# Optimization experiments

Hardware: AMD Instinct MI355X
Metric: run time of the kernel (lower is better)

The kernel has to match this reference:

```python
import jax, jax.numpy as jnp
import numpy as np

B, S, E, H, WIN = 2, 2048, 1024, 16, 16
D = E // H  # head dim = 64


def setup_inputs() -> dict:
    key = jax.random.key(0)
    ks = jax.random.split(key, 9)
    s = 0.02
    f32 = jnp.float32
    return {
        "hidden_states": jax.random.normal(ks[0], (B, S, E), f32),
        "in_w_cls": jax.random.normal(ks[1], (3 * E, E), f32) * s,
        "in_b_cls": jnp.zeros((3 * E,), f32),
        "out_w_cls": jax.random.normal(ks[2], (E, E), f32) * s,
        "out_b_cls": jnp.zeros((E,), f32),
        "in_w_loc": jax.random.normal(ks[3], (3 * E, E), f32) * s,
        "in_b_loc": jnp.zeros((3 * E,), f32),
        "out_w_loc": jax.random.normal(ks[4], (E, E), f32) * s,
        "out_b_loc": jnp.zeros((E,), f32),
    }


def reference(hidden_states, in_w_cls, in_b_cls, out_w_cls, out_b_cls,
              in_w_loc, in_b_loc, out_w_loc, out_b_loc):
    b, s, e = hidden_states.shape
    sq = s - 1
    scale = 1.0 / np.sqrt(D)

    # ---------- global CLS attention: CLS token attends to all tokens ----------
    wq, wk, wv = jnp.split(in_w_cls, 3, axis=0)   # each [E, E]
    bq, bk, bv = jnp.split(in_b_cls, 3, axis=0)
    q = (hidden_states[:, 0:1] @ wq.T + bq).reshape(b, 1, H, D)
    k = (hidden_states @ wk.T + bk).reshape(b, s, H, D)
    v = (hidden_states @ wv.T + bv).reshape(b, s, H, D)
    scores = jnp.einsum('bqhd,bkhd->bhqk', q * scale, k)      # [b,H,1,s]
    attn = jax.nn.softmax(scores, axis=-1)
    ctx = jnp.einsum('bhqk,bkhd->bqhd', attn, v).reshape(b, 1, e)
    global_out = ctx @ out_w_cls.T + out_b_cls                # [b,1,E]

    # ---------- local window attention for tokens 1..s-1 ----------
    wq, wk, wv = jnp.split(in_w_loc, 3, axis=0)
    bq, bk, bv = jnp.split(in_b_loc, 3, axis=0)
    Q = (hidden_states[:, 1:] @ wq.T + bq).reshape(b, sq, H, D)
    K = (hidden_states @ wk.T + bk).reshape(b, s, H, D)
    V = (hidden_states @ wv.T + bv).reshape(b, s, H, D)

    qpos = jnp.arange(1, s)                                   # [sq]
    offs = jnp.arange(-WIN, WIN + 1)                          # [W]
    kidx = qpos[:, None] + offs[None, :]                      # [sq, W]
    valid = (kidx >= 1) & (kidx < s)                          # token 0 excluded
    kidx_c = jnp.clip(kidx, 0, s - 1)

    Kw = K[:, kidx_c]                                         # [b,sq,W,H,D]
    Vw = V[:, kidx_c]
    scores = jnp.einsum('bqhd,bqwhd->bhqw', Q * scale, Kw)    # [b,H,sq,W]
    scores = jnp.where(valid[None, None, :, :], scores, -1e30)
    attn = jax.nn.softmax(scores, axis=-1)
    ctx = jnp.einsum('bhqw,bqwhd->bqhd', attn, Vw).reshape(b, sq, e)
    local_out = ctx @ out_w_loc.T + out_b_loc                 # [b,sq,E]

    return jnp.concatenate([global_out, local_out], axis=1)   # [b,s,E]
```

## Files before the change

### kernel.cpp

```cpp
#include <hip/hip_runtime.h>

#define BB 2
#define SS 2048
#define EE 1024
#define HH 16
#define DD 64
#define NY 5120

typedef __attribute__((ext_vector_type(8))) short short8;
typedef __attribute__((ext_vector_type(4))) float f32x4;

__device__ __forceinline__ float bf2f(unsigned short u) {
  union { unsigned int i; float f; } v; v.i = ((unsigned int)u) << 16; return v.f;
}
__device__ __forceinline__ unsigned short f2bf(float f) {
  unsigned int u = __float_as_uint(f);
  u += 0x7fff + ((u >> 16) & 1);
  return (unsigned short)(u >> 16);
}
__device__ __forceinline__ void gload_lds16(const void* g, void* l) {
  __builtin_amdgcn_global_load_lds(
      (const __attribute__((address_space(1))) void*)g,
      (__attribute__((address_space(3))) void*)l, 16, 0, 0);
}

__global__ void cast_all(const float* __restrict__ s0, unsigned short* __restrict__ d0,
                         const float* __restrict__ s1, unsigned short* __restrict__ d1,
                         const float* __restrict__ s2, unsigned short* __restrict__ d2,
                         const float* __restrict__ s3, unsigned short* __restrict__ d3,
                         const float* __restrict__ in_w_cls,
                         const float* __restrict__ in_b_cls,
                         float* __restrict__ qcls) {
  int b = blockIdx.x;
  if (b >= 10240) {
    int gw = (b - 10240) * 4 + (threadIdx.x >> 6);
    int lane = threadIdx.x & 63;
    int bb = gw >> 10, n = gw & 1023;
    const float* x = s0 + (size_t)bb * SS * EE;
    const float* w = in_w_cls + (size_t)n * EE;
    float s = 0.0f;
    for (int k = lane; k < EE; k += 64) s += x[k] * w[k];
    for (int o = 32; o; o >>= 1) s += __shfl_xor(s, o);
    if (lane == 0) qcls[bb * EE + n] = s + in_b_cls[n];
    return;
  }
  const float* s; unsigned short* d; int idx;
  if (b < 4096)      { s = s0; d = d0; idx = b; }
  else if (b < 6144) { s = s1; d = d1; idx = b - 4096; }
  else if (b < 9216) { s = s2; d = d2; idx = b - 6144; }
  else               { s = s3; d = d3; idx = b - 9216; }
  int i = (idx * 256 + threadIdx.x) * 4;
  float4 v = *reinterpret_cast<const float4*>(s + i);
  ushort4 o;
  o.x = f2bf(v.x); o.y = f2bf(v.y); o.z = f2bf(v.z); o.w = f2bf(v.w);
  *reinterpret_cast<ushort4*>(d + i) = o;
}

#define SBAR __builtin_amdgcn_sched_barrier(0)
#define RAWBAR do { SBAR; __builtin_amdgcn_s_barrier(); SBAR; } while (0)
#define WAITVM0 do { asm volatile("s_waitcnt vmcnt(0)" ::: "memory"); SBAR; } while (0)
#define LGKM0 do { asm volatile("s_waitcnt lgkmcnt(0)" ::: "memory"); SBAR; } while (0)
#define LGKMW(n) do { asm volatile("s_waitcnt lgkmcnt(" #n ")" ::: "memory"); SBAR; } while (0)

#define MFMA20(FAX, MH)                                                              \
  _Pragma("unroll")                                                                  \
  for (int m = 0; m < 4; ++m)                                                        \
    _Pragma("unroll")                                                                \
    for (int n = 0; n < 5; ++n)                                                      \
      acc[(MH) * 4 + m][n] = __builtin_amdgcn_mfma_f32_16x16x32_bf16(                \
          FAX[m], bfr[n], acc[(MH) * 4 + m][n], 0, 0, 0);

__global__ __launch_bounds__(512)
void gemm8p(const unsigned short* __restrict__ Ag,
            const unsigned short* __restrict__ Bg,
            const float* __restrict__ bcls,
            const float* __restrict__ bloc,
            unsigned short* __restrict__ Yout) {
  __shared__ unsigned short As2[2][256][64];
  __shared__ unsigned short Bs2[2][320][64];
  char* ldsA = (char*)As2;
  char* ldsB = (char*)Bs2;

  const int tid = threadIdx.x;
  const int wid = tid >> 6;
  const int lane = tid & 63;
  const int wm = wid >> 2;
  const int wn = wid & 3;
  const int rl = lane & 15;
  const int g4 = lane >> 4;

  int bid = blockIdx.x;
  bid = (bid & 7) * 32 + (bid >> 3);
  const int tileM = (bid & 15) * 256;
  const int tileN = (bid >> 4) * 320;

  f32x4 acc[8][5] = {};
  short8 FA0[4], FA1[4], bfr[5];

  auto SA = [&](int c, int kk, int i) {
    int flat = i * 8192 + tid * 16;
    int row = flat >> 7;
    int colb = (flat & 127) ^ ((row & 7) << 4);
    gload_lds16(Ag + (size_t)(tileM + row) * 1024 + kk + (colb >> 1),
                ldsA + c * 32768 + i * 8192 + wid * 1024);
  };
  auto SB = [&](int c, int kk, int j) {
    int flat = j * 8192 + tid * 16;
    int row = flat >> 7;
    int colb = (flat & 127) ^ ((row & 7) << 4);
    gload_lds16(Bg + (size_t)(tileN + row) * 1024 + kk + (colb >> 1),
                ldsB + c * 40960 + j * 8192 + wid * 1024);
  };
  auto DSA = [&](int c, int mh, int kh, short8* dst) {
#pragma unroll
    for (int m = 0; m < 4; ++m) {
      int row = wm * 128 + mh * 64 + m * 16 + rl;
      const char* base = ldsA + c * 32768 + row * 128;
      dst[m] = *(const short8*)(base + ((kh * 64 + g4 * 16) ^ ((row & 7) << 4)));
    }
  };
  auto DSB = [&](int c, int kh) {
#pragma unroll
    for (int n = 0; n < 5; ++n) {
      int row = wn * 80 + n * 16 + rl;
      const char* base = ldsB + c * 40960 + row * 128;
      bfr[n] = *(const short8*)(base + ((kh * 64 + g4 * 16) ^ ((row & 7) << 4)));
    }
  };

  SA(0, 0, 0); SA(0, 0, 1); SA(0, 0, 2); SA(0, 0, 3);
  SB(0, 0, 0); SB(0, 0, 1); SB(0, 0, 2); SB(0, 0, 3); SB(0, 0, 4);
  WAITVM0;
  RAWBAR;
  DSB(0, 0); DSA(0, 0, 0, FA0);

#pragma unroll 1
  for (int t = 0; t < 16; ++t) {
    const int c = t & 1;
    const int kk = (t + 1) * 64;
    const bool st = (t < 15);
    DSA(c, 1, 0, FA1);
    if (st) { SA(c ^ 1, kk, 0); SA(c ^ 1, kk, 1); }
    RAWBAR; LGKMW(4);
    __builtin_amdgcn_s_setprio(1); MFMA20(FA0, 0); __builtin_amdgcn_s_setprio(0);
    RAWBAR;
    DSA(c, 0, 1, FA0);
    if (st) { SA(c ^ 1, kk, 2); SA(c ^ 1, kk, 3); }
    RAWBAR; LGKMW(4);
    __builtin_amdgcn_s_setprio(1); MFMA20(FA1, 1); __builtin_amdgcn_s_setprio(0);
    RAWBAR;
    DSB(c, 1); DSA(c, 1, 1, FA1);
    if (st) { SB(c ^ 1, kk, 0); SB(c ^ 1, kk, 1); SB(c ^ 1, kk, 2); }
    RAWBAR; LGKM0;
    __builtin_amdgcn_s_setprio(1); MFMA20(FA0, 0); __builtin_amdgcn_s_setprio(0);
    RAWBAR;
    if (st) { SB(c ^ 1, kk, 3); SB(c ^ 1, kk, 4); }
    RAWBAR;
    __builtin_amdgcn_s_setprio(1); MFMA20(FA1, 1); __builtin_amdgcn_s_setprio(0);
    if (st) WAITVM0;
    RAWBAR;
    if (st) { DSB(c ^ 1, 0); DSA(c ^ 1, 0, 0, FA0); }
  }

#pragma unroll
  for (int m = 0; m < 8; ++m)
#pragma unroll
    for (int n = 0; n < 5; ++n) {
      int gc = tileN + wn * 80 + n * 16 + rl;
      float bv = (gc < 2048) ? bcls[1024 + gc] : bloc[gc - 2048];
#pragma unroll
      for (int r = 0; r < 4; ++r) {
        int gr = tileM + wm * 128 + m * 16 + g4 * 4 + r;
        Yout[(size_t)gr * NY + gc] = f2bf(acc[m][n][r] + bv);
      }
    }
}

__global__ __launch_bounds__(256, 4)
void gemm_out(const unsigned short* __restrict__ A,
              const unsigned short* __restrict__ B,
              const float* __restrict__ bias0,
              float* __restrict__ C,
              const float* __restrict__ part,
              const float* __restrict__ Wc,
              const float* __restrict__ bc) {
  __shared__ unsigned short As[2][128 * 32];
  __shared__ unsigned short Bs[2][128 * 32];
  __shared__ float ctx[EE];
  __shared__ float u[HH][8];

  const int tid = threadIdx.x;

  if (blockIdx.x >= 256) {
    const int cid = blockIdx.x - 256;
    const int b = cid >> 8;
    const float* pb = part + (size_t)b * HH * 8 * 66;
    if (tid < HH) {
      const float* pp = pb + tid * 8 * 66;
      float M = -1e30f;
#pragma unroll
      for (int i = 0; i < 8; ++i) M = fmaxf(M, pp[i * 66]);
      float Z = 0.0f, w[8];
#pragma unroll
      for (int i = 0; i < 8; ++i) { w[i] = __expf(pp[i * 66] - M); Z += w[i] * pp[i * 66 + 1]; }
#pragma unroll
      for (int i = 0; i < 8; ++i) u[tid][i] = w[i] / Z;
    }
    __syncthreads();
    for (int k = tid; k < EE; k += 256) {
      int hh = k >> 6, d = k & 63;
      const float* pp = pb + hh * 8 * 66 + 2 + d;
      float a = 0.0f;
#pragma unroll
      for (int i = 0; i < 8; ++i) a += u[hh][i] * pp[i * 66];
      ctx[k] = a;
    }
    __syncthreads();
    int n = (cid & 255) * 4 + (tid >> 6);
    int lane = tid & 63;
    const float* w = Wc + (size_t)n * EE;
    float s = 0.0f;
    for (int k = lane; k < EE; k += 64) s += ctx[k] * w[k];
    for (int o = 32; o; o >>= 1) s += __shfl_xor(s, o);
    if (lane == 0) C[(size_t)b * SS * EE + n] = s + bc[n];
    return;
  }

  const int wid = tid >> 6;
  const int lane = tid & 63;
  int bid = blockIdx.x;
  bid = (bid & 7) * 32 + (bid >> 3);
  const int tileM = (bid % 32) * 128;
  const int tileN = (bid / 32) * 128;

  const int wm = (wid >> 1) * 64;
  const int wn = (wid & 1) * 64;
  const int rl = lane & 15;
  const int kc = (lane >> 4) * 8;

  f32x4 acc[4][4] = {};

  const int srow = tid >> 2;
  const int scol = (tid & 3) * 8;
  const unsigned short* gA = A + (size_t)(tileM + srow) * EE + scol;
  const unsigned short* gB = B + (size_t)(tileN + srow) * EE + scol;
  char* lA = (char*)As + wid * 1024;
  char* lB = (char*)Bs + wid * 1024;

  auto STAGE = [&](int buf, int k0) {
    gload_lds16(gA + k0, lA + buf * 8192);
    gload_lds16(gA + (size_t)64 * EE + k0, lA + buf * 8192 + 4096);
    gload_lds16(gB + k0, lB + buf * 8192);
    gload_lds16(gB + (size_t)64 * EE + k0, lB + buf * 8192 + 4096);
  };
  auto COMPUTE = [&](int buf) {
    const unsigned short* as = As[buf];
    const unsigned short* bs = Bs[buf];
    short8 af[4], bfg[4];
#pragma unroll
    for (int mi = 0; mi < 4; ++mi)
      af[mi] = *reinterpret_cast<const short8*>(&as[(wm + mi * 16 + rl) * 32 + kc]);
#pragma unroll
    for (int ni = 0; ni < 4; ++ni)
      bfg[ni] = *reinterpret_cast<const short8*>(&bs[(wn + ni * 16 + rl) * 32 + kc]);
#pragma unroll
    for (int mi = 0; mi < 4; ++mi)
#pragma unroll
      for (int ni = 0; ni < 4; ++ni)
        acc[mi][ni] = __builtin_amdgcn_mfma_f32_16x16x32_bf16(
            af[mi], bfg[ni], acc[mi][ni], 0, 0, 0);
  };

  STAGE(0, 0);
  asm volatile("s_waitcnt vmcnt(0)" ::: "memory");
  __syncthreads();
  int cur = 0;
  for (int k0 = 32; k0 < EE; k0 += 32) {
    STAGE(cur ^ 1, k0);
    COMPUTE(cur);
    asm volatile("s_waitcnt vmcnt(0)" ::: "memory");
    __syncthreads();
    cur ^= 1;
  }
  COMPUTE(cur);

  const int crow0 = (lane >> 4) * 4;
  const int ccol = lane & 15;
#pragma unroll
  for (int mi = 0; mi < 4; ++mi)
#pragma unroll
    for (int ni = 0; ni < 4; ++ni) {
      int gc = tileN + wn + ni * 16 + ccol;
      float bv = bias0[gc];
#pragma unroll
      for (int r = 0; r < 4; ++r) {
        int gr = tileM + wm + mi * 16 + crow0 + r;
        if (gr & 2047)
          C[(size_t)gr * EE + gc] = acc[mi][ni][r] + bv;
      }
    }
}

#define QBL 128
#define VT_PAD 168
#define P_PAD 72
__global__ __launch_bounds__(256, 2)
void attn_fused(const float* __restrict__ qcls,
                const unsigned short* __restrict__ Y,
                float* __restrict__ part,
                unsigned short* __restrict__ CTX) {
  const int h = blockIdx.y, b = blockIdx.z;
  const int tid = threadIdx.x, wid = tid >> 6, lane = tid & 63;

  __shared__ unsigned short Vt[64][VT_PAD];
  __shared__ unsigned short Pl[4][32][P_PAD];
  __shared__ float qf[64];
  __shared__ float ps[256];
  __shared__ float red[8];
  __shared__ float pacc[4][64];

  if (blockIdx.x >= 16) {
    const int kc = blockIdx.x - 16;
    if (tid < 64) qf[tid] = qcls[b * EE + h * DD + tid];
    __syncthreads();

    const int sl = tid >> 3, oct = tid & 7;
    float d8[8];
#pragma unroll
    for (int it = 0; it < 8; ++it) {
      int key = sl + it * 32;
      short8 kv = *(const short8*)&Y[(size_t)(b * SS + kc * 256 + key) * NY + h * DD + oct * 8];
      float d = 0.0f;
#pragma unroll
      for (int e = 0; e < 8; ++e) d += qf[oct * 8 + e] * bf2f((unsigned short)kv[e]);
      d8[it] = d;
    }
#pragma unroll
    for (int it = 0; it < 8; ++it) {
      d8[it] += __shfl_xor(d8[it], 1);
      d8[it] += __shfl_xor(d8[it], 2);
      d8[it] += __shfl_xor(d8[it], 4);
    }
    if (oct == 0) {
#pragma unroll
      for (int it = 0; it < 8; ++it) ps[sl + it * 32] = d8[it] * 0.125f;
    }
    __syncthreads();

    float dot = ps[tid];
    float mx = dot;
    for (int o = 32; o; o >>= 1) mx = fmaxf(mx, __shfl_xor(mx, o));
    if ((tid & 63) == 0) red[tid >> 6] = mx;
    __syncthreads();
    float M = fmaxf(fmaxf(red[0], red[1]), fmaxf(red[2], red[3]));

    float p = __expf(dot - M);
    ps[tid] = p;
    float l = p;
    for (int o = 32; o; o >>= 1) l += __shfl_xor(l, o);
    if ((tid & 63) == 0) red[4 + (tid >> 6)] = l;
    __syncthreads();
    float L = red[4] + red[5] + red[6] + red[7];

    float a8[8] = {0.f, 0.f, 0.f, 0.f, 0.f, 0.f, 0.f, 0.f};
#pragma unroll
    for (int it = 0; it < 8; ++it) {
      int slv = (tid >> 3) + it * 32;
      float p2 = ps[slv];
      short8 v = *(const short8*)&Y[(size_t)(b * SS + kc * 256 + slv) * NY + 1024 + h * DD + oct * 8];
#pragma unroll
      for (int e = 0; e < 8; ++e) a8[e] += p2 * bf2f((unsigned short)v[e]);
    }
#pragma unroll
    for (int e = 0; e < 8; ++e) {
      a8[e] += __shfl_xor(a8[e], 8);
      a8[e] += __shfl_xor(a8[e], 16);
      a8[e] += __shfl_xor(a8[e], 32);
    }
    if (lane < 8) {
#pragma unroll
      for (int e = 0; e < 8; ++e) pacc[wid][lane * 8 + e] = a8[e];
    }
    __syncthreads();
    if (tid < 64) {
      float a = pacc[0][tid] + pacc[1][tid] + pacc[2][tid] + pacc[3][tid];
      float* pp = part + ((size_t)(b * HH + h) * 8 + kc) * 66;
      if (tid == 0) { pp[0] = M; pp[1] = L; }
      pp[2 + tid] = a;
    }
    return;
  }

  const int s0 = blockIdx.x * QBL;
  const int rl = lane & 15, g = lane >> 4;

  for (int task = tid; task < 1280; task += 256) {
    int row = task >> 3, oc = task & 7;
    int kg = min(max(s0 - 16 + row, 0), SS - 1);
    short8 v = *(const short8*)&Y[(size_t)(b * SS + kg) * NY + 4096 + h * DD + oc * 8];
#pragma unroll
    for (int e = 0; e < 8; ++e) Vt[oc * 8 + e][row] = (unsigned short)v[e];
  }
  __syncthreads();

  const int qb = s0 + wid * 32;
  const int kb = qb - 16;

  short8 ak[4][2];
#pragma unroll
  for (int kt = 0; kt < 4; ++kt) {
    int kg = min(max(kb + kt * 16 + rl, 0), SS - 1);
    const unsigned short* kr = &Y[(size_t)(b * SS + kg) * NY + 3072 + h * DD + g * 8];
#pragma unroll
    for (int ks = 0; ks < 2; ++ks) ak[kt][ks] = *(const short8*)(kr + ks * 32);
  }
  short8 bq[2][2];
#pragma unroll
  for (int cc = 0; cc < 2; ++cc) {
    const unsigned short* qr = &Y[(size_t)(b * SS + qb + cc * 16 + rl) * NY + 2048 + h * DD + g * 8];
#pragma unroll
    for (int ks = 0; ks < 2; ++ks) bq[cc][ks] = *(const short8*)(qr + ks * 32);
  }

  f32x4 accs[4][2] = {};
#pragma unroll
  for (int kt = 0; kt < 4; ++kt)
#pragma unroll
    for (int cc = 0; cc < 2; ++cc)
#pragma unroll
      for (int ks = 0; ks < 2; ++ks)
        accs[kt][cc] = __builtin_amdgcn_mfma_f32_16x16x32_bf16(
            ak[kt][ks], bq[cc][ks], accs[kt][cc], 0, 0, 0);

  float mrow[2] = {-3e38f, -3e38f};
#pragma unroll
  for (int kt = 0; kt < 4; ++kt)
#pragma unroll
    for (int cc = 0; cc < 2; ++cc)
#pragma unroll
      for (int r = 0; r < 4; ++r) {
        int kg = kb + kt * 16 + 4 * g + r;
        int qg = qb + cc * 16 + rl;
        bool valid = (kg >= qg - 16) && (kg <= qg + 16) && (kg >= 1) && (kg < SS);
        float v = valid ? accs[kt][cc][r] : -3e38f;
        accs[kt][cc][r] = v;
        mrow[cc] = fmaxf(mrow[cc], v);
      }
#pragma unroll
  for (int cc = 0; cc < 2; ++cc) {
    float m = mrow[cc];
    m = fmaxf(m, __shfl_xor(m, 16));
    m = fmaxf(m, __shfl_xor(m, 32));
    mrow[cc] = m;
  }

  float zrow[2] = {0.0f, 0.0f};
#pragma unroll
  for (int cc = 0; cc < 2; ++cc)
#pragma unroll
    for (int kt = 0; kt < 4; ++kt) {
      ushort4 pw;
#pragma unroll
      for (int r = 0; r < 4; ++r) {
        float p = __expf((accs[kt][cc][r] - mrow[cc]) * 0.125f);
        zrow[cc] += p;
        ((unsigned short*)&pw)[r] = f2bf(p);
      }
      *(ushort4*)&Pl[wid][cc * 16 + rl][kt * 16 + 4 * g] = pw;
    }
#pragma unroll
  for (int cc = 0; cc < 2; ++cc) {
    float z = zrow[cc];
    z += __shfl_xor(z, 16);
    z += __shfl_xor(z, 32);
    zrow[cc] = 1.0f / z;
  }

  f32x4 accp[4][2] = {};
#pragma unroll
  for (int ks = 0; ks < 2; ++ks) {
    short8 bp[2];
#pragma unroll
    for (int cc = 0; cc < 2; ++cc)
      bp[cc] = *(const short8*)&Pl[wid][cc * 16 + rl][ks * 32 + g * 8];
#pragma unroll
    for (int mt = 0; mt < 4; ++mt) {
      short8 av = *(const short8*)&Vt[mt * 16 + rl][wid * 32 + ks * 32 + g * 8];
#pragma unroll
      for (int cc = 0; cc < 2; ++cc)
        accp[mt][cc] = __builtin_amdgcn_mfma_f32_16x16x32_bf16(
            av, bp[cc], accp[mt][cc], 0, 0, 0);
    }
  }

#pragma unroll
  for (int mt = 0; mt < 4; ++mt)
#pragma unroll
    for (int cc = 0; cc < 2; ++cc) {
      int token = qb + cc * 16 + rl;
      if (token == 0) {
        *(ushort4*)&CTX[(size_t)(b * SS) * EE + h * DD + mt * 16 + 4 * g] = ushort4{0, 0, 0, 0};
        continue;
      }
      ushort4 o;
#pragma unroll
      for (int r = 0; r < 4; ++r)
        ((unsigned short*)&o)[r] = f2bf(accp[mt][cc][r] * zrow[cc]);
      *(ushort4*)&CTX[(size_t)(b * SS + token) * EE + h * DD + mt * 16 + 4 * g] = o;
    }
}

extern "C" void kernel_launch(void* const* d_in, const int* in_sizes, int n_in,
                              void* d_out, int out_size, void* d_ws, size_t ws_size,
                              hipStream_t stream) {
  const float* hs        = (const float*)d_in[0];
  const float* in_w_cls  = (const float*)d_in[1];
  const float* in_b_cls  = (const float*)d_in[2];
  const float* out_w_cls = (const float*)d_in[3];
  const float* out_b_cls = (const float*)d_in[4];
  const float* in_w_loc  = (const float*)d_in[5];
  const float* in_b_loc  = (const float*)d_in[6];
  const float* out_w_loc = (const float*)d_in[7];
  const float* out_b_loc = (const float*)d_in[8];
  float* out = (float*)d_out;

  const int M = BB * SS;
  char* ws = (char*)d_ws;
  size_t off = 0;
  auto alloc = [&](size_t bytes) { char* p = ws + off; off += (bytes + 255) & ~(size_t)255; return p; };
  unsigned short* Xbf  = (unsigned short*)alloc((size_t)M * EE * 2);
  unsigned short* W    = (unsigned short*)alloc((size_t)NY * EE * 2);
  unsigned short* Wout = (unsigned short*)alloc((size_t)EE * EE * 2);
  unsigned short* Yb   = (unsigned short*)alloc((size_t)M * NY * 2);
  unsigned short* CTX  = (unsigned short*)alloc((size_t)M * EE * 2);
  float* qcls = (float*)alloc(2 * EE * 4);
  float* part = (float*)alloc((size_t)BB * HH * 8 * 66 * 4);

  cast_all<<<10752, 256, 0, stream>>>(
      hs, Xbf,
      in_w_cls + (size_t)EE * EE, W,
      in_w_loc, W + (size_t)2048 * EE,
      out_w_loc, Wout,
      in_w_cls, in_b_cls, qcls);

  gemm8p<<<256, 512, 0, stream>>>(Xbf, W, in_b_cls, in_b_loc, Yb);

  attn_fused<<<dim3(24, HH, BB), 256, 0, stream>>>(qcls, Yb, part, CTX);

  gemm_out<<<768, 256, 0, stream>>>(CTX, Wout, out_b_loc, out,
                                    part, out_w_cls, out_b_cls);
}
```

Before: 102.6 us.

## Restructure output GEMM with BK=64 swizzled LDS and split-phase pipelining

Measured after the change: 100.5 us. -2.0%, faster.

```diff
diff --git a/kernel.cpp b/kernel.cpp
--- a/kernel.cpp
+++ b/kernel.cpp
@@ -176,7 +176,7 @@
     }
 }
 
-__global__ __launch_bounds__(256, 4)
+__global__ __launch_bounds__(256)
 void gemm_out(const unsigned short* __restrict__ A,
               const unsigned short* __restrict__ B,
               const float* __restrict__ bias0,
@@ -184,10 +184,12 @@
               const float* __restrict__ part,
               const float* __restrict__ Wc,
               const float* __restrict__ bc) {
-  __shared__ unsigned short As[2][128 * 32];
-  __shared__ unsigned short Bs[2][128 * 32];
+  __shared__ unsigned short As2[2][128][64];
+  __shared__ unsigned short Bs2[2][128][64];
   __shared__ float ctx[EE];
   __shared__ float u[HH][8];
+  char* ldsA = (char*)As2;
+  char* ldsB = (char*)Bs2;
 
   const int tid = threadIdx.x;
 
@@ -233,70 +235,90 @@
   const int tileM = (bid % 32) * 128;
   const int tileN = (bid / 32) * 128;
 
-  const int wm = (wid >> 1) * 64;
-  const int wn = (wid & 1) * 64;
+  const int wm = wid >> 1;
+  const int wn = wid & 1;
   const int rl = lane & 15;
-  const int kc = (lane >> 4) * 8;
+  const int g4 = lane >> 4;
 
   f32x4 acc[4][4] = {};
-
-  const int srow = tid >> 2;
-  const int scol = (tid & 3) * 8;
-  const unsigned short* gA = A + (size_t)(tileM + srow) * EE + scol;
-  const unsigned short* gB = B + (size_t)(tileN + srow) * EE + scol;
-  char* lA = (char*)As + wid * 1024;
-  char* lB = (char*)Bs + wid * 1024;
-
-  auto STAGE = [&](int buf, int k0) {
-    gload_lds16(gA + k0, lA + buf * 8192);
-    gload_lds16(gA + (size_t)64 * EE + k0, lA + buf * 8192 + 4096);
-    gload_lds16(gB + k0, lB + buf * 8192);
-    gload_lds16(gB + (size_t)64 * EE + k0, lB + buf * 8192 + 4096);
-  };
-  auto COMPUTE = [&](int buf) {
-    const unsigned short* as = As[buf];
-    const unsigned short* bs = Bs[buf];
-    short8 af[4], bfg[4];
-#pragma unroll
-    for (int mi = 0; mi < 4; ++mi)
-      af[mi] = *reinterpret_cast<const short8*>(&as[(wm + mi * 16 + rl) * 32 + kc]);
-#pragma unroll
-    for (int ni = 0; ni < 4; ++ni)
-      bfg[ni] = *reinterpret_cast<const short8*>(&bs[(wn + ni * 16 + rl) * 32 + kc]);
-#pragma unroll
-    for (int mi = 0; mi < 4; ++mi)
-#pragma unroll
-      for (int ni = 0; ni < 4; ++ni)
-        acc[mi][ni] = __builtin_amdgcn_mfma_f32_16x16x32_bf16(
-            af[mi], bfg[ni], acc[mi][ni], 0, 0, 0);
-  };
-
-  STAGE(0, 0);
-  asm volatile("s_waitcnt vmcnt(0)" ::: "memory");
-  __syncthreads();
-  int cur = 0;
-  for (int k0 = 32; k0 < EE; k0 += 32) {
-    STAGE(cur ^ 1, k0);
-    COMPUTE(cur);
-    asm volatile("s_waitcnt vmcnt(0)" ::: "memory");
-    __syncthreads();
-    cur ^= 1;
-  }
-  COMPUTE(cur);
-
-  const int crow0 = (lane >> 4) * 4;
-  const int ccol = lane & 15;
-#pragma unroll
-  for (int mi = 0; mi < 4; ++mi)
-#pragma unroll
-    for (int ni = 0; ni < 4; ++ni) {
-      int gc = tileN + wn + ni * 16 + ccol;
+  short8 FA0[4], FA1[4], FB0[4], FB1[4];
+
+  auto SA2 = [&](int c, int kk, int i) {
+    int flat = i * 4096 + tid * 16;
+    int row = flat >> 7;
+    int colb = (flat & 127) ^ ((row & 7) << 4);
+    gload_lds16(A + (size_t)(tileM + row) * EE + kk + (colb >> 1),
+                ldsA + c * 16384 + i * 4096 + wid * 1024);
+  };
+  auto SB2 = [&](int c, int kk, int i) {
+    int flat = i * 4096 + tid * 16;
+    int row = flat >> 7;
+    int colb = (flat & 127) ^ ((row & 7) << 4);
+    gload_lds16(B + (size_t)(tileN + row) * EE + kk + (colb >> 1),
+                ldsB + c * 16384 + i * 4096 + wid * 1024);
+  };
+  auto RDA = [&](int c, int kh, short8* dst) {
+#pragma unroll
+    for (int m = 0; m < 4; ++m) {
+      int row = wm * 64 + m * 16 + rl;
+      const char* base = ldsA + c * 16384 + row * 128;
+      dst[m] = *(const short8*)(base + ((kh * 64 + g4 * 16) ^ ((row & 7) << 4)));
+    }
+  };
+  auto RDB = [&](int c, int kh, short8* dst) {
+#pragma unroll
+    for (int n = 0; n < 4; ++n) {
+      int row = wn * 64 + n * 16 + rl;
+      const char* base = ldsB + c * 16384 + row * 128;
+      dst[n] = *(const short8*)(base + ((kh * 64 + g4 * 16) ^ ((row & 7) << 4)));
+    }
+  };
+  auto MF16 = [&](short8* fa, short8* fb) {
+    __builtin_amdgcn_s_setprio(1);
+#pragma unroll
+    for (int m = 0; m < 4; ++m)
+#pragma unroll
+      for (int n = 0; n < 4; ++n)
+        acc[m][n] = __builtin_amdgcn_mfma_f32_16x16x32_bf16(
+            fa[m], fb[n], acc[m][n], 0, 0, 0);
+    __builtin_amdgcn_s_setprio(0);
+  };
+
+  SA2(0, 0, 0); SA2(0, 0, 1); SA2(0, 0, 2); SA2(0, 0, 3);
+  SB2(0, 0, 0); SB2(0, 0, 1); SB2(0, 0, 2); SB2(0, 0, 3);
+  WAITVM0;
+  RAWBAR;
+  RDA(0, 0, FA0); RDB(0, 0, FB0);
+
+#pragma unroll 1
+  for (int t = 0; t < 16; ++t) {
+    const int c = t & 1;
+    const int kk = (t + 1) * 64;
+    const bool st = (t < 15);
+    RDA(c, 1, FA1); RDB(c, 1, FB1);
+    if (st) { SA2(c ^ 1, kk, 0); SA2(c ^ 1, kk, 1); SA2(c ^ 1, kk, 2); SA2(c ^ 1, kk, 3); }
+    RAWBAR; LGKMW(8);
+    MF16(FA0, FB0);
+    RAWBAR;
+    if (st) { SB2(c ^ 1, kk, 0); SB2(c ^ 1, kk, 1); SB2(c ^ 1, kk, 2); SB2(c ^ 1, kk, 3); }
+    RAWBAR; LGKM0;
+    MF16(FA1, FB1);
+    if (st) WAITVM0;
+    RAWBAR;
+    if (st) { RDA(c ^ 1, 0, FA0); RDB(c ^ 1, 0, FB0); }
+  }
+
+#pragma unroll
+  for (int m = 0; m < 4; ++m)
+#pragma unroll
+    for (int n = 0; n < 4; ++n) {
+      int gc = tileN + wn * 64 + n * 16 + rl;
       float bv = bias0[gc];
 #pragma unroll
       for (int r = 0; r < 4; ++r) {
-        int gr = tileM + wm + mi * 16 + crow0 + r;
+        int gr = tileM + wm * 64 + m * 16 + g4 * 4 + r;
         if (gr & 2047)
-          C[(size_t)gr * EE + gc] = acc[mi][ni][r] + bv;
+          C[(size_t)gr * EE + gc] = acc[m][n][r] + bv;
       }
     }
 }
```
